# Kernel optimization log

Measured on AMD Instinct MI355X. Metric: run time of the kernel, lower is better.

## Reference

```python
import jax, jax.numpy as jnp
import numpy as np

N = 50000   # total nodes
D = 128     # feature dim
E = 800000  # edges (avg degree 16)
G = 100     # graphs (500 nodes each)


def setup_inputs() -> dict:
    key = jax.random.key(0)
    ks = jax.random.split(key, 9)
    s = 1.0 / np.sqrt(D)
    X = jax.random.normal(ks[0], (N, D), jnp.float32)
    src = jax.random.randint(ks[1], (E,), 0, N)
    dst = jax.random.randint(ks[2], (E,), 0, N)
    edge_index = jnp.stack([src, dst])  # [2, E]
    edge_weight = jax.random.uniform(ks[3], (E,), jnp.float32)
    # 100 graphs of 500 nodes each (graph_sizes = [500]*100)
    segment_ids = jnp.repeat(jnp.arange(G), N // G)
    return {
        "X": X,
        "edge_weight": edge_weight,
        "W1": jax.random.normal(ks[4], (D, D), jnp.float32) * s,
        "b1": jnp.zeros((D,), jnp.float32),
        "W2": jax.random.normal(ks[5], (D, D), jnp.float32) * s,
        "b2": jnp.zeros((D,), jnp.float32),
        "Wf": jax.random.normal(ks[6], (D, 1), jnp.float32) * s,
        "bf": jnp.zeros((1,), jnp.float32),
        "edge_index": edge_index,
        "segment_ids": segment_ids,
    }


def gcn_conv(X, edge_index, edge_weight, W, b):
    # h_v = sum_{(u->v)} w_e * (X @ W)[u] + b   (sparse A @ XW)
    h = X @ W                                   # [N, d_out]
    msgs = h[edge_index[0]] * edge_weight[:, None]  # [E, d_out]
    agg = jax.ops.segment_sum(msgs, edge_index[1], num_segments=N)
    return agg + b


def reference(X, edge_weight, W1, b1, W2, b2, Wf, bf, edge_index, segment_ids):
    # layer stack: conv -> relu -> dropout(eval=identity)
    h = jax.nn.relu(gcn_conv(X, edge_index, edge_weight, W1, b1))
    h = jax.nn.relu(gcn_conv(h, edge_index, edge_weight, W2, b2))
    out = jax.nn.sigmoid(gcn_conv(h, edge_index, edge_weight, Wf, bf))  # [N, 1]
    # fused per-graph mean readout (replaces split(graph_sizes) python loop)
    sums = jax.ops.segment_sum(out.sum(axis=1), segment_ids, num_segments=G)
    counts = jax.ops.segment_sum(jnp.ones((N,), out.dtype), segment_ids, num_segments=G)
    return sums / (counts * out.shape[1])  # [G]
```

## Files before the change

kernel.cpp:

```cpp
#include <hip/hip_runtime.h>
#include <hip/hip_fp16.h>

#define N_NODES 50000
#define DIM 128
#define NEDGE 800000
#define NGRAPH 100
#define NPG 500
#define NBUCKET 250
#define NPB 200
#define BCAP 4096
#define CHUNK 4096
#define EPT (CHUNK / 256)
#define SCAT_BLK ((NEDGE + CHUNK - 1) / CHUNK)

typedef _Float16 f16x8 __attribute__((ext_vector_type(8)));
typedef float f32x4 __attribute__((ext_vector_type(4)));
typedef float f32x2 __attribute__((ext_vector_type(2)));

__device__ inline float wgt(unsigned p) {
    return __half2float(__ushort_as_half((unsigned short)(p & 0xffffu)));
}
__device__ inline void accrow(uint2 q, float w, float* acc) {
    f32x2 f;
    f = __builtin_amdgcn_cvt_pk_f32_fp8((int)q.x, false); acc[0] = fmaf(w, f[0], acc[0]); acc[1] = fmaf(w, f[1], acc[1]);
    f = __builtin_amdgcn_cvt_pk_f32_fp8((int)q.x, true);  acc[2] = fmaf(w, f[0], acc[2]); acc[3] = fmaf(w, f[1], acc[3]);
    f = __builtin_amdgcn_cvt_pk_f32_fp8((int)q.y, false); acc[4] = fmaf(w, f[0], acc[4]); acc[5] = fmaf(w, f[1], acc[5]);
    f = __builtin_amdgcn_cvt_pk_f32_fp8((int)q.y, true);  acc[6] = fmaf(w, f[0], acc[6]); acc[7] = fmaf(w, f[1], acc[7]);
}

__global__ void scatter_prep(const int* __restrict__ src, const int* __restrict__ dst,
                             const float* __restrict__ w, int* __restrict__ gCur,
                             uint2* __restrict__ stage, const float* __restrict__ W1,
                             const float* __restrict__ W2, _Float16* __restrict__ fragW1,
                             _Float16* __restrict__ fragW2, int E) {
    if (blockIdx.x >= SCAT_BLK) {
        const int b = blockIdx.x - SCAT_BLK;
        const float* W = (b < 64) ? W1 : W2;
        _Float16* F = (b < 64) ? fragW1 : fragW2;
        int idx = (b & 63) * 256 + threadIdx.x;
        int j = idx & 7, l = (idx >> 3) & 63, kt = (idx >> 9) & 3, nt = idx >> 11;
        int k = kt * 32 + ((l >> 4) << 3) + j;
        int col = (nt << 4) + (l & 15);
        F[idx] = (_Float16)W[k * DIM + col];
        return;
    }
    __shared__ int hist[NBUCKET];
    __shared__ int base[NBUCKET];
    for (int i = threadIdx.x; i < NBUCKET; i += 256) hist[i] = 0;
    __syncthreads();
    const int e0 = blockIdx.x * CHUNK;
    int myDst[EPT];
#pragma unroll
    for (int j = 0; j < EPT; ++j) {
        int e = e0 + j * 256 + threadIdx.x;
        int d = (e < E) ? dst[e] : -1;
        myDst[j] = d;
        if (d >= 0) atomicAdd(&hist[d / NPB], 1);
    }
    __syncthreads();
    for (int i = threadIdx.x; i < NBUCKET; i += 256)
        base[i] = i * BCAP + atomicAdd(&gCur[i], hist[i]);
    __syncthreads();
#pragma unroll
    for (int j = 0; j < EPT; ++j) {
        int d = myDst[j];
        if (d >= 0) {
            int e = e0 + j * 256 + threadIdx.x;
            int b = d / NPB;
            int p = atomicAdd(&base[b], 1);
            unsigned short wh = __half_as_ushort(__float2half_rn(w[e]));
            stage[p] = make_uint2(((unsigned)src[e] << 16) | (unsigned)wh,
                                  (unsigned)(d - b * NPB));
        }
    }
}

__device__ inline f16x8 load_afrag_f32(const float* a) {
    float4 u0 = *(const float4*)a;
    float4 u1 = *(const float4*)(a + 4);
    f16x8 r;
    r[0] = (_Float16)u0.x; r[1] = (_Float16)u0.y; r[2] = (_Float16)u0.z; r[3] = (_Float16)u0.w;
    r[4] = (_Float16)u1.x; r[5] = (_Float16)u1.y; r[6] = (_Float16)u1.z; r[7] = (_Float16)u1.w;
    return r;
}

__device__ inline void gemm_tile_f32(const float* __restrict__ A, const _Float16* fragW,
                                     unsigned char* __restrict__ C, int blk, int tid) {
    const int lane = tid & 63;
    const int wid = tid >> 6;
    const int row0 = blk * 128 + wid * 16;
    if (row0 >= N_NODES) return;
    const int arow = row0 + (lane & 15);
    const int koff = (lane >> 4) << 3;
    f32x4 acc[8] = {};
#pragma unroll
    for (int kt = 0; kt < 4; ++kt) {
        f16x8 a = load_afrag_f32(A + (size_t)arow * DIM + kt * 32 + koff);
#pragma unroll
        for (int nt = 0; nt < 8; ++nt) {
            f16x8 b = *(const f16x8*)&fragW[(((nt << 2) | kt) << 9) | (lane << 3)];
            acc[nt] = __builtin_amdgcn_mfma_f32_16x16x32_f16(a, b, acc[nt], 0, 0, 0);
        }
    }
    const int crow = row0 + ((lane >> 4) << 2);
    const int ccol = lane & 15;
#pragma unroll
    for (int nt = 0; nt < 8; ++nt) {
#pragma unroll
        for (int r = 0; r < 4; ++r) {
            int v8 = __builtin_amdgcn_cvt_pk_fp8_f32(acc[nt][r], acc[nt][r], 0, false);
            C[(size_t)(crow + r) * DIM + (nt << 4) + ccol] = (unsigned char)(v8 & 0xff);
        }
    }
}

#define MFMA_BLK ((N_NODES + 127) / 128)
__global__ __launch_bounds__(512) void gemm1_build(
        const float* __restrict__ A, const _Float16* __restrict__ fragWg,
        unsigned char* __restrict__ C, const int* __restrict__ gCur,
        const uint2* __restrict__ stage, unsigned int* __restrict__ pack,
        int2* __restrict__ range) {
    __shared__ __align__(16) _Float16 fragW[16384];
    __shared__ int lhist[NPB];
    __shared__ int lincl[256];
    __shared__ int lcur[NPB];
    const int tid = threadIdx.x;
    if (blockIdx.x < MFMA_BLK) {
        for (int i = tid; i < 2048; i += 512)
            ((uint4*)fragW)[i] = ((const uint4*)fragWg)[i];
        __syncthreads();
        gemm_tile_f32(A, fragW, C, blockIdx.x, tid);
        return;
    }
    const int b = blockIdx.x - MFMA_BLK;
    const int t = tid;
    const int cnt = gCur[b];
    for (int i = t; i < NPB; i += 512) lhist[i] = 0;
    __syncthreads();
    unsigned myX[BCAP / 512];
    int myLd[BCAP / 512];
#pragma unroll
    for (int j = 0; j < BCAP / 512; ++j) {
        int i = j * 512 + t;
        if (i < cnt) {
            uint2 r = stage[b * BCAP + i];
            myX[j] = r.x;
            myLd[j] = (int)r.y;
            atomicAdd(&lhist[r.y], 1);
        } else {
            myLd[j] = -1;
        }
    }
    __syncthreads();
    int h = (t < NPB) ? lhist[t] : 0;
    if (t < 256) lincl[t] = h;
    __syncthreads();
    for (int off = 1; off < 256; off <<= 1) {
        int v = (t >= off && t < 256) ? lincl[t - off] : 0;
        __syncthreads();
        if (t < 256) lincl[t] += v;
        __syncthreads();
    }
    if (t < NPB) lcur[t] = lincl[t] - h;
    __syncthreads();
#pragma unroll
    for (int j = 0; j < BCAP / 512; ++j) {
        if (myLd[j] >= 0) {
            int p = atomicAdd(&lcur[myLd[j]], 1);
            pack[b * BCAP + p] = myX[j];
        }
    }
    if (t < NPB) {
        int v = b * NPB + t;
        range[v] = make_int2(b * BCAP + lincl[t] - h, b * BCAP + lincl[t]);
    }
}

__global__ __launch_bounds__(256) void gather_gemm2(
        const unsigned char* __restrict__ msg, const unsigned int* __restrict__ pack,
        const int2* __restrict__ range, const float* __restrict__ bias,
        const _Float16* __restrict__ fragW2, unsigned char* __restrict__ C) {
    __shared__ __align__(16) char hT[16 * 256];
    const int t = threadIdx.x;
    const int grpL = t >> 4;
    const int lane16 = t & 15;
    const int tile = blockIdx.x;
    {
        const int grp = tile * 16 + grpL;
        int2 r = range[grp];
        int beg = r.x, end = r.y;
        float acc[8] = {};
        int i = beg;
        for (; i + 7 < end; i += 8) {
            unsigned p[8];
            uint2 q[8];
#pragma unroll
            for (int j = 0; j < 8; ++j) p[j] = pack[i + j];
#pragma unroll
            for (int j = 0; j < 8; ++j)
                q[j] = ((const uint2*)(msg + (size_t)(p[j] >> 16) * DIM))[lane16];
#pragma unroll
            for (int j = 0; j < 8; ++j) accrow(q[j], wgt(p[j]), acc);
        }
        for (; i + 3 < end; i += 4) {
            unsigned p0 = pack[i], p1 = pack[i + 1], p2 = pack[i + 2], p3 = pack[i + 3];
            uint2 q0 = ((const uint2*)(msg + (size_t)(p0 >> 16) * DIM))[lane16];
            uint2 q1 = ((const uint2*)(msg + (size_t)(p1 >> 16) * DIM))[lane16];
            uint2 q2 = ((const uint2*)(msg + (size_t)(p2 >> 16) * DIM))[lane16];
            uint2 q3 = ((const uint2*)(msg + (size_t)(p3 >> 16) * DIM))[lane16];
            accrow(q0, wgt(p0), acc);
            accrow(q1, wgt(p1), acc);
            accrow(q2, wgt(p2), acc);
            accrow(q3, wgt(p3), acc);
        }
        for (; i < end; ++i) {
            unsigned p = pack[i];
            uint2 q = ((const uint2*)(msg + (size_t)(p >> 16) * DIM))[lane16];
            accrow(q, wgt(p), acc);
        }
        float4 b0 = ((const float4*)bias)[2 * lane16];
        float4 b1 = ((const float4*)bias)[2 * lane16 + 1];
        union { __half2 h[4]; uint4 u; } o;
        o.h[0] = __floats2half2_rn(fmaxf(acc[0] + b0.x, 0.f), fmaxf(acc[1] + b0.y, 0.f));
        o.h[1] = __floats2half2_rn(fmaxf(acc[2] + b0.z, 0.f), fmaxf(acc[3] + b0.w, 0.f));
        o.h[2] = __floats2half2_rn(fmaxf(acc[4] + b1.x, 0.f), fmaxf(acc[5] + b1.y, 0.f));
        o.h[3] = __floats2half2_rn(fmaxf(acc[6] + b1.z, 0.f), fmaxf(acc[7] + b1.w, 0.f));
        int boff = (grpL << 8) | (lane16 << 4);
        boff ^= (grpL & 7) << 4;
        *(uint4*)(hT + boff) = o.u;
    }
    __syncthreads();
    const int lane = t & 63;
    const int wid = t >> 6;
    const int arowL = lane & 15;
    const int koff = (lane >> 4) << 3;
    f32x4 acc2[2] = {};
#pragma unroll
    for (int kt = 0; kt < 4; ++kt) {
        int boff = (arowL << 8) | ((kt * 32 + koff) << 1);
        boff ^= (arowL & 7) << 4;
        f16x8 a = *(const f16x8*)(hT + boff);
#pragma unroll
        for (int n = 0; n < 2; ++n) {
            int nt = wid * 2 + n;
            f16x8 b = *(const f16x8*)&fragW2[(((nt << 2) | kt) << 9) | (lane << 3)];
            acc2[n] = __builtin_amdgcn_mfma_f32_16x16x32_f16(a, b, acc2[n], 0, 0, 0);
        }
    }
    const int crow = tile * 16 + ((lane >> 4) << 2);
    const int ccol = lane & 15;
#pragma unroll
    for (int n = 0; n < 2; ++n) {
#pragma unroll
        for (int r = 0; r < 4; ++r) {
            int v8 = __builtin_amdgcn_cvt_pk_fp8_f32(acc2[n][r], acc2[n][r], 0, false);
            C[(size_t)(crow + r) * DIM + ((wid * 2 + n) << 4) + ccol] = (unsigned char)(v8 & 0xff);
        }
    }
}

__global__ void gather_wf(const unsigned char* __restrict__ msg,
                          const unsigned int* __restrict__ pack,
                          const int2* __restrict__ range, const float* __restrict__ bias,
                          const float* __restrict__ wf, float* __restrict__ outS) {
    int gid = blockIdx.x * blockDim.x + threadIdx.x;
    int grp = gid >> 4, lane = gid & 15;
    if (grp >= N_NODES) return;
    int2 r = range[grp];
    int beg = r.x, end = r.y;
    float acc[8] = {};
    int i = beg;
    for (; i + 7 < end; i += 8) {
        unsigned p[8];
        uint2 q[8];
#pragma unroll
        for (int j = 0; j < 8; ++j) p[j] = pack[i + j];
#pragma unroll
        for (int j = 0; j < 8; ++j)
            q[j] = ((const uint2*)(msg + (size_t)(p[j] >> 16) * DIM))[lane];
#pragma unroll
        for (int j = 0; j < 8; ++j) accrow(q[j], wgt(p[j]), acc);
    }
    for (; i + 3 < end; i += 4) {
        unsigned p0 = pack[i], p1 = pack[i + 1], p2 = pack[i + 2], p3 = pack[i + 3];
        uint2 q0 = ((const uint2*)(msg + (size_t)(p0 >> 16) * DIM))[lane];
        uint2 q1 = ((const uint2*)(msg + (size_t)(p1 >> 16) * DIM))[lane];
        uint2 q2 = ((const uint2*)(msg + (size_t)(p2 >> 16) * DIM))[lane];
        uint2 q3 = ((const uint2*)(msg + (size_t)(p3 >> 16) * DIM))[lane];
        accrow(q0, wgt(p0), acc);
        accrow(q1, wgt(p1), acc);
        accrow(q2, wgt(p2), acc);
        accrow(q3, wgt(p3), acc);
    }
    for (; i < end; ++i) {
        unsigned p = pack[i];
        uint2 q = ((const uint2*)(msg + (size_t)(p >> 16) * DIM))[lane];
        accrow(q, wgt(p), acc);
    }
    float4 b0 = ((const float4*)bias)[2 * lane];
    float4 b1 = ((const float4*)bias)[2 * lane + 1];
    float4 f0 = ((const float4*)wf)[2 * lane];
    float4 f1 = ((const float4*)wf)[2 * lane + 1];
    float d = fmaxf(acc[0] + b0.x, 0.f) * f0.x + fmaxf(acc[1] + b0.y, 0.f) * f0.y
            + fmaxf(acc[2] + b0.z, 0.f) * f0.z + fmaxf(acc[3] + b0.w, 0.f) * f0.w
            + fmaxf(acc[4] + b1.x, 0.f) * f1.x + fmaxf(acc[5] + b1.y, 0.f) * f1.y
            + fmaxf(acc[6] + b1.z, 0.f) * f1.z + fmaxf(acc[7] + b1.w, 0.f) * f1.w;
#pragma unroll
    for (int off = 8; off; off >>= 1) d += __shfl_down(d, off, 16);
    if (lane == 0) outS[grp] = d;
}

__global__ void final_readout(const float* __restrict__ s, const unsigned int* __restrict__ pack,
                              const int2* __restrict__ range, const float* __restrict__ bfp,
                              float* __restrict__ out) {
    __shared__ float red[256];
    int g = blockIdx.x;
    float bf = bfp[0];
    float sum = 0.f;
    for (int n = threadIdx.x; n < NPG; n += blockDim.x) {
        int v = g * NPG + n;
        int2 r = range[v];
        float a = 0.f;
        for (int i = r.x; i < r.y; ++i) {
            unsigned int p = pack[i];
            a += wgt(p) * s[p >> 16];
        }
        a += bf;
        sum += 1.f / (1.f + expf(-a));
    }
    red[threadIdx.x] = sum;
    __syncthreads();
    for (int t = 128; t > 0; t >>= 1) {
        if (threadIdx.x < t) red[threadIdx.x] += red[threadIdx.x + t];
        __syncthreads();
    }
    if (threadIdx.x == 0) out[g] = red[0] / (float)NPG;
}

extern "C" void kernel_launch(void* const* d_in, const int* in_sizes, int n_in,
                              void* d_out, int out_size, void* d_ws, size_t ws_size,
                              hipStream_t stream) {
    const float* X  = (const float*)d_in[0];
    const float* ew = (const float*)d_in[1];
    const float* W1 = (const float*)d_in[2];
    const float* b1 = (const float*)d_in[3];
    const float* W2 = (const float*)d_in[4];
    const float* b2 = (const float*)d_in[5];
    const float* Wf = (const float*)d_in[6];
    const float* bf = (const float*)d_in[7];
    const int* ei   = (const int*)d_in[8];
    const int* src  = ei;
    const int* dst  = ei + NEDGE;

    float* out = (float*)d_out;

    char* ws = (char*)d_ws;
    size_t off = 0;
    unsigned char* bufA = (unsigned char*)(ws + off); off += (size_t)N_NODES * DIM;
    unsigned char* bufB = (unsigned char*)(ws + off); off += (size_t)N_NODES * DIM;
    uint2* stage = (uint2*)(ws + off);  off += (size_t)NBUCKET * BCAP * 8;
    unsigned int* pack = (unsigned int*)(ws + off); off += (size_t)NBUCKET * BCAP * 4;
    int2* range = (int2*)(ws + off);    off += (size_t)N_NODES * 8;
    int* gCur   = (int*)(ws + off);     off += (size_t)256 * 4;
    _Float16* fragW1 = (_Float16*)(ws + off); off += (size_t)16384 * 2;
    _Float16* fragW2 = (_Float16*)(ws + off); off += (size_t)16384 * 2;
    float* s_node = (float*)(ws + off); off += (size_t)N_NODES * 4;

    const int TB = 256;
    const int TILE_BLK = N_NODES / 16;
    const int GATHER_BLK = (N_NODES * 16 + TB - 1) / TB;

    hipMemsetAsync(gCur, 0, (size_t)NBUCKET * 4, stream);
    scatter_prep<<<SCAT_BLK + 128, TB, 0, stream>>>(src, dst, ew, gCur, stage,
                                                    W1, W2, fragW1, fragW2, NEDGE);
    gemm1_build<<<MFMA_BLK + NBUCKET, 512, 0, stream>>>(X, fragW1, bufA, gCur,
                                                        stage, pack, range);
    gather_gemm2<<<TILE_BLK, TB, 0, stream>>>(bufA, pack, range, b1, fragW2, bufB);
    gather_wf<<<GATHER_BLK, TB, 0, stream>>>(bufB, pack, range, b2, Wf, s_node);
    final_readout<<<NGRAPH, TB, 0, stream>>>(s_node, pack, range, bf, out);
}
```

Before: 100.5 us.

## Sort nodes by in-degree per bucket to balance gather work in wavefronts

In the CSR build kernel, each bucket's 200 nodes are counting-sorted by in-degree (capped at 63) into a nodeOrder permutation. The two gather kernels then process nodes in this order, so the 16-lane groups sharing a wavefront or tile have similar edge counts and less divergence in their loop trip counts. Outputs are scattered back to the original node rows through the permutation. The cost is an extra indirection load, scattered output row writes, and a serial prefix scan on thread 0 per bucket.

```diff
diff --git a/kernel.cpp b/kernel.cpp
--- a/kernel.cpp
+++ b/kernel.cpp
@@ -119,11 +119,13 @@
         const float* __restrict__ A, const _Float16* __restrict__ fragWg,
         unsigned char* __restrict__ C, const int* __restrict__ gCur,
         const uint2* __restrict__ stage, unsigned int* __restrict__ pack,
-        int2* __restrict__ range) {
+        int2* __restrict__ range, int* __restrict__ nodeOrder) {
     __shared__ __align__(16) _Float16 fragW[16384];
     __shared__ int lhist[NPB];
     __shared__ int lincl[256];
     __shared__ int lcur[NPB];
+    __shared__ int dh[64];
+    __shared__ int dcur[64];
     const int tid = threadIdx.x;
     if (blockIdx.x < MFMA_BLK) {
         for (int i = tid; i < 2048; i += 512)
@@ -174,19 +176,36 @@
         int v = b * NPB + t;
         range[v] = make_int2(b * BCAP + lincl[t] - h, b * BCAP + lincl[t]);
     }
+    if (t < 64) dh[t] = 0;
+    __syncthreads();
+    int deg = 0;
+    if (t < NPB) { deg = min(h, 63); atomicAdd(&dh[deg], 1); }
+    __syncthreads();
+    if (t == 0) {
+        int run = 0;
+        for (int d2 = 0; d2 < 64; ++d2) { int c = dh[d2]; dcur[d2] = run; run += c; }
+    }
+    __syncthreads();
+    if (t < NPB) {
+        int slot = atomicAdd(&dcur[deg], 1);
+        nodeOrder[b * NPB + slot] = b * NPB + t;
+    }
 }
 
 __global__ __launch_bounds__(256) void gather_gemm2(
         const unsigned char* __restrict__ msg, const unsigned int* __restrict__ pack,
-        const int2* __restrict__ range, const float* __restrict__ bias,
-        const _Float16* __restrict__ fragW2, unsigned char* __restrict__ C) {
+        const int2* __restrict__ range, const int* __restrict__ nodeOrder,
+        const float* __restrict__ bias, const _Float16* __restrict__ fragW2,
+        unsigned char* __restrict__ C) {
     __shared__ __align__(16) char hT[16 * 256];
+    __shared__ int sh_node[16];
     const int t = threadIdx.x;
     const int grpL = t >> 4;
     const int lane16 = t & 15;
     const int tile = blockIdx.x;
     {
-        const int grp = tile * 16 + grpL;
+        const int grp = nodeOrder[tile * 16 + grpL];
+        if (lane16 == 0) sh_node[grpL] = grp;
         int2 r = range[grp];
         int beg = r.x, end = r.y;
         float acc[8] = {};
@@ -247,25 +266,28 @@
             acc2[n] = __builtin_amdgcn_mfma_f32_16x16x32_f16(a, b, acc2[n], 0, 0, 0);
         }
     }
-    const int crow = tile * 16 + ((lane >> 4) << 2);
+    const int lrow0 = ((lane >> 4) << 2);
     const int ccol = lane & 15;
 #pragma unroll
     for (int n = 0; n < 2; ++n) {
 #pragma unroll
         for (int r = 0; r < 4; ++r) {
+            int node = sh_node[lrow0 + r];
             int v8 = __builtin_amdgcn_cvt_pk_fp8_f32(acc2[n][r], acc2[n][r], 0, false);
-            C[(size_t)(crow + r) * DIM + ((wid * 2 + n) << 4) + ccol] = (unsigned char)(v8 & 0xff);
+            C[(size_t)node * DIM + ((wid * 2 + n) << 4) + ccol] = (unsigned char)(v8 & 0xff);
         }
     }
 }
 
 __global__ void gather_wf(const unsigned char* __restrict__ msg,
                           const unsigned int* __restrict__ pack,
-                          const int2* __restrict__ range, const float* __restrict__ bias,
+                          const int2* __restrict__ range, const int* __restrict__ nodeOrder,
+                          const float* __restrict__ bias,
                           const float* __restrict__ wf, float* __restrict__ outS) {
     int gid = blockIdx.x * blockDim.x + threadIdx.x;
-    int grp = gid >> 4, lane = gid & 15;
-    if (grp >= N_NODES) return;
+    int idx = gid >> 4, lane = gid & 15;
+    if (idx >= N_NODES) return;
+    int grp = nodeOrder[idx];
     int2 r = range[grp];
     int beg = r.x, end = r.y;
     float acc[8] = {};
@@ -361,6 +383,7 @@
     uint2* stage = (uint2*)(ws + off);  off += (size_t)NBUCKET * BCAP * 8;
     unsigned int* pack = (unsigned int*)(ws + off); off += (size_t)NBUCKET * BCAP * 4;
     int2* range = (int2*)(ws + off);    off += (size_t)N_NODES * 8;
+    int* nodeOrder = (int*)(ws + off);  off += (size_t)N_NODES * 4;
     int* gCur   = (int*)(ws + off);     off += (size_t)256 * 4;
     _Float16* fragW1 = (_Float16*)(ws + off); off += (size_t)16384 * 2;
     _Float16* fragW2 = (_Float16*)(ws + off); off += (size_t)16384 * 2;
@@ -374,8 +397,10 @@
     scatter_prep<<<SCAT_BLK + 128, TB, 0, stream>>>(src, dst, ew, gCur, stage,
                                                     W1, W2, fragW1, fragW2, NEDGE);
     gemm1_build<<<MFMA_BLK + NBUCKET, 512, 0, stream>>>(X, fragW1, bufA, gCur,
-                                                        stage, pack, range);
-    gather_gemm2<<<TILE_BLK, TB, 0, stream>>>(bufA, pack, range, b1, fragW2, bufB);
-    gather_wf<<<GATHER_BLK, TB, 0, stream>>>(bufB, pack, range, b2, Wf, s_node);
+                                                        stage, pack, range, nodeOrder);
+    gather_gemm2<<<TILE_BLK, TB, 0, stream>>>(bufA, pack, range, nodeOrder, b1,
+                                              fragW2, bufB);
+    gather_wf<<<GATHER_BLK, TB, 0, stream>>>(bufB, pack, range, nodeOrder, b2,
+                                             Wf, s_node);
     final_readout<<<NGRAPH, TB, 0, stream>>>(s_node, pack, range, bf, out);
 }
```

New measurement: 100.6 us. About the same (+0.1%).
